# Kernel optimization log

Measured on AMD Instinct MI355X. Metric: run time of the kernel, lower is better.

## Reference

```python
import jax, jax.numpy as jnp
import numpy as np

B, T, D = 2, 1024, 2048
N, K, H = 16, 4, 128          # num_heads, num_kv_heads, head_dim
TC = 1024                     # cached tokens
S = TC + T
MAX_WAVELENGTH = 10000.0
BIG_NEG = -2.3819763e38


def _apply_rope(x, positions):
    """RoPE: positions [B,L] applied to x [B,L,heads,H]."""
    half = x.shape[-1] // 2
    freq_exponents = (2.0 / x.shape[-1]) * jnp.arange(half, dtype=jnp.float32)
    timescale = MAX_WAVELENGTH ** freq_exponents                      # [H/2]
    radians = (positions.astype(jnp.float32)[..., None] / timescale)[..., None, :]  # [B,L,1,H/2]
    sin, cos = jnp.sin(radians), jnp.cos(radians)
    x1, x2 = jnp.split(x, 2, axis=-1)
    res = jnp.concatenate([x1 * cos - x2 * sin, x2 * cos + x1 * sin], axis=-1)
    return res.astype(x.dtype)


def setup_inputs() -> dict:
    key = jax.random.key(0)
    ks = jax.random.split(key, 8)
    x = jax.random.normal(ks[0], (B, T, D), dtype=jnp.float32)
    # new tokens sit right after the cache
    positions = jnp.broadcast_to(TC + jnp.arange(T, dtype=jnp.int32), (B, T))
    # causal mask over [cache + new]: query t may attend to keys s <= TC + t
    s_idx = jnp.arange(S)[None, :]
    t_idx = jnp.arange(T)[:, None]
    attn_mask = jnp.broadcast_to((s_idx <= TC + t_idx)[None, None, :, :], (B, 1, T, S))
    cache_k = jax.random.normal(ks[1], (B, TC, K, H), dtype=jnp.float32)
    cache_v = jax.random.normal(ks[2], (B, TC, K, H), dtype=jnp.float32)
    # lecun-normal-ish fan-in scaling (fan_in = D for projections, N*H for output)
    w_q = jax.random.normal(ks[3], (N, D, H), dtype=jnp.float32) * (D ** -0.5)
    w_kv = jax.random.normal(ks[4], (2, K, D, H), dtype=jnp.float32) * (D ** -0.5)
    w_out = jax.random.normal(ks[5], (N, H, D), dtype=jnp.float32) * ((N * H) ** -0.5)
    return {"x": x, "positions": positions, "attn_mask": attn_mask,
            "cache_k": cache_k, "cache_v": cache_v,
            "w_q": w_q, "w_kv": w_kv, "w_out": w_out}


def reference(x, positions, attn_mask, cache_k, cache_v, w_q, w_kv, w_out):
    dtype = x.dtype
    # projections (GQA path: num_kv_heads != num_heads)
    q = jnp.einsum('BTD,NDH->BTNH', x, w_q.astype(dtype))
    kv = jnp.einsum('BSD,CKDH->CBSKH', x, w_kv.astype(dtype))
    k_new, v_new = kv[0], kv[1]
    # inline RoPE + query scaling
    q = _apply_rope(q, positions) * (H ** -0.5)
    k_new = _apply_rope(k_new, positions)
    # KV-cache concat
    k = jnp.concatenate([cache_k, k_new], axis=1)   # [B,S,K,H]
    v = jnp.concatenate([cache_v, v_new], axis=1)
    # group heads: B T (K G) H -> B T K G H
    G = N // K
    qg = q.reshape(q.shape[0], q.shape[1], K, G, H)
    logits = jnp.einsum('BTKGH,BSKH->BKGTS', qg, k,
                        preferred_element_type=jnp.float32)
    masked = jnp.where(attn_mask[:, :, None, :, :], logits, BIG_NEG)
    probs = jax.nn.softmax(masked, axis=-1).astype(dtype)
    enc = jnp.einsum('BKGTS,BSKH->BTKGH', probs, v)
    enc = enc.reshape(enc.shape[0], enc.shape[1], N, H)  # B T (K G) H
    out = jnp.einsum('BTNH,NHD->BTD', enc, w_out.astype(dtype))
    return out, k, v
```

## Files before the change

### kernel.cpp

```cpp
#include <hip/hip_runtime.h>

#define B_  2
#define T_  1024
#define D_  2048
#define NH  16
#define KH  4
#define HD  128
#define TC_ 1024
#define S_  2048

typedef __bf16 bf16x4v __attribute__((ext_vector_type(4)));
typedef __bf16 bf16x8v __attribute__((ext_vector_type(8)));
typedef float  f32x4v  __attribute__((ext_vector_type(4)));

__device__ __forceinline__ void async_copy16(void* lds, const void* g) {
    __builtin_amdgcn_global_load_lds(
        (__attribute__((address_space(1))) void*)g,
        (__attribute__((address_space(3))) void*)lds, 16, 0, 0);
}

__global__ void cvt_x(const float* __restrict__ x, __bf16* __restrict__ xb) {
    int i = (blockIdx.x * 256 + threadIdx.x) * 4;
    float4 v = *(const float4*)(x + i);
    bf16x4v o; o[0]=(__bf16)v.x; o[1]=(__bf16)v.y; o[2]=(__bf16)v.z; o[3]=(__bf16)v.w;
    *(bf16x4v*)(xb + i) = o;
}

__global__ void tp_w(const float* __restrict__ in, __bf16* __restrict__ out) {
    __shared__ float tile[32][33];
    int h0 = blockIdx.x * 32;
    int d0 = blockIdx.y * 32;
    const float* ip = in + (size_t)blockIdx.z * (D_ * HD);
    __bf16* op = out + (size_t)blockIdx.z * (D_ * HD);
    int tx = threadIdx.x, ty = threadIdx.y;
    for (int i = 0; i < 32; i += 8)
        tile[ty + i][tx] = ip[(size_t)(d0 + ty + i) * HD + h0 + tx];
    __syncthreads();
    for (int i = 0; i < 32; i += 8)
        op[(size_t)(h0 + ty + i) * D_ + d0 + tx] = (__bf16)tile[tx][ty + i];
}

__global__ void tp_wout(const float* __restrict__ in, __bf16* __restrict__ out) {
    __shared__ float tile[32][33];
    int d0 = blockIdx.x * 32;
    int h0 = blockIdx.y * 32;
    int n  = blockIdx.z;
    const float* ip = in + (size_t)n * (HD * D_);
    int tx = threadIdx.x, ty = threadIdx.y;
    for (int i = 0; i < 32; i += 8)
        tile[ty + i][tx] = ip[(size_t)(h0 + ty + i) * D_ + d0 + tx];
    __syncthreads();
    for (int i = 0; i < 32; i += 8)
        out[(size_t)(d0 + ty + i) * (NH * HD) + n * HD + h0 + tx] = (__bf16)tile[tx][ty + i];
}

__global__ void tp_v(const float* __restrict__ vout, __bf16* __restrict__ vtb) {
    __shared__ float tile[32][33];
    int z = blockIdx.z; int b = z / KH, kh = z % KH;
    int h0 = blockIdx.x * 32;
    int s0 = blockIdx.y * 32;
    const float* ip = vout + ((size_t)b * S_ * KH + kh) * HD;
    int tx = threadIdx.x, ty = threadIdx.y;
    for (int i = 0; i < 32; i += 8)
        tile[ty + i][tx] = ip[(size_t)(s0 + ty + i) * (KH * HD) + h0 + tx];
    __syncthreads();
    __bf16* op = vtb + ((size_t)b * KH + kh) * (size_t)HD * S_;
    for (int i = 0; i < 32; i += 8)
        op[(size_t)(h0 + ty + i) * S_ + s0 + tx] = (__bf16)tile[tx][ty + i];
}

__global__ void copy_cache(const float4* __restrict__ ck, const float4* __restrict__ cv,
                           float* __restrict__ kout, float* __restrict__ vout,
                           __bf16* __restrict__ kb) {
    int i = blockIdx.x * 256 + threadIdx.x;
    int b = i >> 17;
    int r = i & 131071;
    float4 kv = ck[i];
    ((float4*)(kout + (size_t)b * S_ * KH * HD))[r] = kv;
    ((float4*)(vout + (size_t)b * S_ * KH * HD))[r] = cv[i];
    int h4 = r & 31;
    int kh = (r >> 5) & 3;
    int s  = r >> 7;
    bf16x4v o; o[0]=(__bf16)kv.x; o[1]=(__bf16)kv.y; o[2]=(__bf16)kv.z; o[3]=(__bf16)kv.w;
    *(bf16x4v*)(kb + (((size_t)(b * KH + kh) * S_ + s) * HD) + h4 * 4) = o;
}

__global__ __launch_bounds__(256, 2)
void gemm_qkv(const __bf16* __restrict__ A, const __bf16* __restrict__ BT,
              const int* __restrict__ pos, __bf16* __restrict__ qws,
              float* __restrict__ kout, float* __restrict__ vout,
              __bf16* __restrict__ kb) {
    __shared__ __bf16 As[128 * 64];
    __shared__ __bf16 Bs[128 * 64];
    const int m0 = blockIdx.x * 128, n0 = blockIdx.y * 128;
    const int tid = threadIdx.x;
    const int wave = tid >> 6, lane = tid & 63;
    const int quad = lane >> 4, l16 = lane & 15;
    const int wm = (wave & 1) * 64;
    const int bn0 = (wave >> 1) * 32;
    const int lrow = lane >> 3;
    const int lsw  = (lane & 7) ^ (lrow & 7);

    f32x4v acc[4][4];
    for (int i = 0; i < 4; i++)
        for (int j = 0; j < 4; j++)
            acc[i][j] = (f32x4v){0.f, 0.f, 0.f, 0.f};

    const __bf16* Abase = A + (size_t)m0 * D_;
    const __bf16* Bbase = BT + (size_t)n0 * D_;

    for (int k0 = 0; k0 < D_; k0 += 64) {
        for (int j = 0; j < 4; j++) {
            int r = wave * 32 + j * 8;
            async_copy16(As + (size_t)r * 64,
                         Abase + (size_t)(r + lrow) * D_ + k0 + lsw * 8);
            async_copy16(Bs + (size_t)r * 64,
                         Bbase + (size_t)(r + lrow) * D_ + k0 + lsw * 8);
        }
        __syncthreads();
        for (int ks = 0; ks < 2; ks++) {
            const int ch = ((ks * 4 + quad) ^ (l16 & 7)) * 8;
            bf16x8v a[4], b[4];
            for (int i = 0; i < 4; i++)
                a[i] = *(const bf16x8v*)(As + (wm + i * 16 + l16) * 64 + ch);
            for (int j = 0; j < 4; j++) {
                int bn = bn0 + (j >> 1) * 16 + (j & 1) * 64;
                b[j] = *(const bf16x8v*)(Bs + (bn + l16) * 64 + ch);
            }
            for (int i = 0; i < 4; i++)
                for (int j = 0; j < 4; j++)
                    acc[i][j] = __builtin_amdgcn_mfma_f32_16x16x32_bf16(a[i], b[j], acc[i][j], 0, 0, 0);
        }
        __syncthreads();
    }

    const float RFREQ = 9.210340371976184f / 64.0f;
    const float qscale = 0.08838834764831845f;
    const int head = blockIdx.y;

    if (head < NH) {
        for (int i = 0; i < 4; i++)
            for (int r = 0; r < 4; r++) {
                int row = m0 + wm + i * 16 + quad * 4 + r;
                float p = (float)pos[row];
                size_t qo = ((size_t)row * NH + head) * HD;
                for (int jp = 0; jp < 2; jp++) {
                    int hh = bn0 + jp * 16 + l16;
                    float ang = p * __expf(-(float)hh * RFREQ);
                    float sn, cs; __sincosf(ang, &sn, &cs);
                    float x1 = acc[i][jp * 2][r], x2 = acc[i][jp * 2 + 1][r];
                    qws[qo + hh]      = (__bf16)((x1 * cs - x2 * sn) * qscale);
                    qws[qo + hh + 64] = (__bf16)((x2 * cs + x1 * sn) * qscale);
                }
            }
    } else if (head < NH + KH) {
        int kh = head - NH;
        for (int i = 0; i < 4; i++)
            for (int r = 0; r < 4; r++) {
                int row = m0 + wm + i * 16 + quad * 4 + r;
                int b = row >> 10, t = row & 1023;
                float p = (float)pos[row];
                size_t ko  = ((size_t)(b * S_ + TC_ + t) * KH + kh) * HD;
                size_t kbo = ((size_t)(b * KH + kh) * S_ + TC_ + t) * HD;
                for (int jp = 0; jp < 2; jp++) {
                    int hh = bn0 + jp * 16 + l16;
                    float ang = p * __expf(-(float)hh * RFREQ);
                    float sn, cs; __sincosf(ang, &sn, &cs);
                    float x1 = acc[i][jp * 2][r], x2 = acc[i][jp * 2 + 1][r];
                    float k1 = x1 * cs - x2 * sn, k2 = x2 * cs + x1 * sn;
                    kout[ko + hh]      = k1;
                    kout[ko + hh + 64] = k2;
                    kb[kbo + hh]      = (__bf16)k1;
                    kb[kbo + hh + 64] = (__bf16)k2;
                }
            }
    } else {
        int kh = head - NH - KH;
        for (int i = 0; i < 4; i++)
            for (int r = 0; r < 4; r++) {
                int row = m0 + wm + i * 16 + quad * 4 + r;
                int b = row >> 10, t = row & 1023;
                size_t vo = ((size_t)(b * S_ + TC_ + t) * KH + kh) * HD;
                for (int j = 0; j < 4; j++) {
                    int h = bn0 + (j >> 1) * 16 + (j & 1) * 64 + l16;
                    vout[vo + h] = acc[i][j][r];
                }
            }
    }
}

__global__ __launch_bounds__(256, 2)
void gemm_bt(const __bf16* __restrict__ A, const __bf16* __restrict__ BT,
             float* __restrict__ C0, float* __restrict__ C1, int ldc, int kchunk) {
    __shared__ __bf16 As[128 * 64];
    __shared__ __bf16 Bs[128 * 64];
    const int m0 = blockIdx.x * 128, n0 = blockIdx.y * 128;
    const int kbeg = blockIdx.z * kchunk;
    float* C = blockIdx.z ? C1 : C0;
    const int tid = threadIdx.x;
    const int wave = tid >> 6, lane = tid & 63;
    const int quad = lane >> 4, l16 = lane & 15;
    const int wm = (wave & 1) * 64, wn = (wave >> 1) * 64;
    const int lrow = lane >> 3;
    const int lsw  = (lane & 7) ^ (lrow & 7);

    f32x4v acc[4][4];
    for (int i = 0; i < 4; i++)
        for (int j = 0; j < 4; j++)
            acc[i][j] = (f32x4v){0.f, 0.f, 0.f, 0.f};

    const __bf16* Abase = A + (size_t)m0 * D_;
    const __bf16* Bbase = BT + (size_t)n0 * D_;

    for (int k0 = kbeg; k0 < kbeg + kchunk; k0 += 64) {
        for (int j = 0; j < 4; j++) {
            int r = wave * 32 + j * 8;
            async_copy16(As + (size_t)r * 64,
                         Abase + (size_t)(r + lrow) * D_ + k0 + lsw * 8);
            async_copy16(Bs + (size_t)r * 64,
                         Bbase + (size_t)(r + lrow) * D_ + k0 + lsw * 8);
        }
        __syncthreads();
        for (int ks = 0; ks < 2; ks++) {
            const int ch = ((ks * 4 + quad) ^ (l16 & 7)) * 8;
            bf16x8v a[4], b[4];
            for (int i = 0; i < 4; i++)
                a[i] = *(const bf16x8v*)(As + (wm + i * 16 + l16) * 64 + ch);
            for (int j = 0; j < 4; j++)
                b[j] = *(const bf16x8v*)(Bs + (wn + j * 16 + l16) * 64 + ch);
            for (int i = 0; i < 4; i++)
                for (int j = 0; j < 4; j++)
                    acc[i][j] = __builtin_amdgcn_mfma_f32_16x16x32_bf16(a[i], b[j], acc[i][j], 0, 0, 0);
        }
        __syncthreads();
    }
    for (int i = 0; i < 4; i++)
        for (int j = 0; j < 4; j++)
            for (int r = 0; r < 4; r++) {
                int row = m0 + wm + i * 16 + quad * 4 + r;
                int col = n0 + wn + j * 16 + l16;
                C[(size_t)row * ldc + col] = acc[i][j][r];
            }
}

__global__ void add2(float* __restrict__ out, const float* __restrict__ p1) {
    int i = blockIdx.x * 256 + threadIdx.x;
    f32x4v a = *(const f32x4v*)(out + (size_t)i * 4);
    f32x4v b = *(const f32x4v*)(p1 + (size_t)i * 4);
    a[0]+=b[0]; a[1]+=b[1]; a[2]+=b[2]; a[3]+=b[3];
    *(f32x4v*)(out + (size_t)i * 4) = a;
}

__global__ __launch_bounds__(512, 1)
void attn(const __bf16* __restrict__ qws, const __bf16* __restrict__ kb,
          const __bf16* __restrict__ vtb, __bf16* __restrict__ enc) {
    __shared__ __bf16 Qs[128 * 128];
    __shared__ __bf16 Ks[128 * 128];
    __shared__ __bf16 Vs[128 * 128];
    __shared__ __bf16 Ps[128 * 128];

    const int t0 = blockIdx.x * 128;
    const int n  = blockIdx.y;
    const int b  = blockIdx.z;
    const int kh = n / (NH / KH);
    const int tid = threadIdx.x, wave = tid >> 6, lane = tid & 63;
    const int quad = lane >> 4, l16 = lane & 15;
    const int wm = wave * 16;
    const int arow = lane >> 4;
    const int acol = lane & 15;

    {
        const __bf16* qtile = qws + ((size_t)(b * T_ + t0) * NH + n) * HD;
        for (int jj = 0; jj < 4; jj++) {
            int r0 = wm + jj * 4;
            int row = r0 + arow;
            async_copy16(Qs + (size_t)r0 * 128,
                         qtile + (size_t)row * (NH * HD) + ((acol ^ (row & 15)) * 8));
        }
    }

    float m_run[4], l_run[4];
    f32x4v o_acc[8];
    for (int r = 0; r < 4; r++) { m_run[r] = -INFINITY; l_run[r] = 0.f; }
    for (int j = 0; j < 8; j++) o_acc[j] = (f32x4v){0.f, 0.f, 0.f, 0.f};

    const int nS = (TC_ + t0 + 128) >> 7;
    const __bf16* kbase = kb  + ((size_t)(b * KH + kh)) * S_ * HD;
    const __bf16* vbase = vtb + ((size_t)(b * KH + kh)) * (size_t)HD * S_;

    for (int st = 0; st < nS; st++) {
        const int s0 = st * 128;
        {
            const __bf16* ktile = kbase + (size_t)s0 * HD;
            for (int jj = 0; jj < 4; jj++) {
                int r0 = wm + jj * 4;
                int row = r0 + arow;
                async_copy16(Ks + (size_t)r0 * 128,
                             ktile + (size_t)row * HD + ((acol ^ (row & 15)) * 8));
            }
        }
        {
            const __bf16* vtile = vbase + s0;
            for (int jj = 0; jj < 4; jj++) {
                int r0 = wm + jj * 4;
                int row = r0 + arow;
                async_copy16(Vs + (size_t)r0 * 128,
                             vtile + (size_t)row * S_ + ((acol ^ (row & 15)) * 8));
            }
        }
        __syncthreads();

        f32x4v sc[8];
        for (int j = 0; j < 8; j++) sc[j] = (f32x4v){0.f, 0.f, 0.f, 0.f};
        for (int ks = 0; ks < 4; ks++) {
            int ch = (ks * 4 + quad) ^ l16;
            bf16x8v a = *(const bf16x8v*)(Qs + (wm + l16) * 128 + ch * 8);
            bf16x8v bb[8];
            for (int j = 0; j < 8; j++)
                bb[j] = *(const bf16x8v*)(Ks + (j * 16 + l16) * 128 + ch * 8);
            for (int j = 0; j < 8; j++)
                sc[j] = __builtin_amdgcn_mfma_f32_16x16x32_bf16(a, bb[j], sc[j], 0, 0, 0);
        }

        if (st == nS - 1) {
            for (int j = 0; j < 8; j++)
                for (int r = 0; r < 4; r++) {
                    int row = wm + quad * 4 + r;
                    int col = j * 16 + l16;
                    if (col > row) sc[j][r] = -3.0e38f;
                }
        }

        for (int r = 0; r < 4; r++) {
            float mx = sc[0][r];
            for (int j = 1; j < 8; j++) mx = fmaxf(mx, sc[j][r]);
            for (int off = 8; off >= 1; off >>= 1) mx = fmaxf(mx, __shfl_xor(mx, off, 64));
            mx = fmaxf(mx, m_run[r]);
            float alpha = __expf(m_run[r] - mx);
            m_run[r] = mx;
            float s = 0.f;
            for (int j = 0; j < 8; j++) {
                float pv = __expf(sc[j][r] - mx);
                sc[j][r] = pv;
                s += pv;
            }
            for (int off = 8; off >= 1; off >>= 1) s += __shfl_xor(s, off, 64);
            l_run[r] = l_run[r] * alpha + s;
            for (int j = 0; j < 8; j++) o_acc[j][r] *= alpha;
        }

        for (int j = 0; j < 8; j++)
            for (int r = 0; r < 4; r++) {
                int row = wm + quad * 4 + r;
                int c = (j * 2 + (l16 >> 3)) ^ (row & 15);
                Ps[row * 128 + c * 8 + (l16 & 7)] = (__bf16)sc[j][r];
            }
        __syncthreads();

        for (int ks = 0; ks < 4; ks++) {
            int ch = (ks * 4 + quad) ^ l16;
            bf16x8v a = *(const bf16x8v*)(Ps + (wm + l16) * 128 + ch * 8);
            bf16x8v bb[8];
            for (int j = 0; j < 8; j++)
                bb[j] = *(const bf16x8v*)(Vs + (j * 16 + l16) * 128 + ch * 8);
            for (int j = 0; j < 8; j++)
                o_acc[j] = __builtin_amdgcn_mfma_f32_16x16x32_bf16(a, bb[j], o_acc[j], 0, 0, 0);
        }
        __syncthreads();
    }

    for (int r = 0; r < 4; r++) {
        float inv = 1.0f / l_run[r];
        int row = wm + quad * 4 + r;
        for (int j = 0; j < 8; j++) {
            int col = j * 16 + l16;
            enc[((size_t)(b * T_ + t0 + row) * NH + n) * HD + col] =
                (__bf16)(o_acc[j][r] * inv);
        }
    }
}

extern "C" void kernel_launch(void* const* d_in, const int* in_sizes, int n_in,
                              void* d_out, int out_size, void* d_ws, size_t ws_size,
                              hipStream_t stream) {
    const float* x       = (const float*)d_in[0];
    const int*   pos     = (const int*)d_in[1];
    const float* cache_k = (const float*)d_in[3];
    const float* cache_v = (const float*)d_in[4];
    const float* w_q     = (const float*)d_in[5];
    const float* w_kv    = (const float*)d_in[6];
    const float* w_out   = (const float*)d_in[7];

    float* out  = (float*)d_out;
    float* kout = out  + (size_t)B_ * T_ * D_;
    float* vout = kout + (size_t)B_ * S_ * KH * HD;

    char* ws = (char*)d_ws;
    __bf16* xb   = (__bf16*)ws;  ws += (size_t)B_ * T_ * D_ * 2;
    __bf16* wt   = (__bf16*)ws;  ws += (size_t)3072 * D_ * 2;
    __bf16* wot  = (__bf16*)ws;  ws += (size_t)D_ * NH * HD * 2;
    float*  op1  = (float*)ws;   ws += (size_t)B_ * T_ * D_ * 4;
    __bf16* qws  = (__bf16*)ws;  ws += (size_t)B_ * T_ * NH * HD * 2;
    __bf16* kbuf = (__bf16*)ws;  ws += (size_t)B_ * S_ * KH * HD * 2;
    __bf16* vtb  = (__bf16*)ws;  ws += (size_t)B_ * S_ * KH * HD * 2;
    __bf16* enc  = (__bf16*)ws;

    cvt_x<<<4096, 256, 0, stream>>>(x, xb);
    tp_w<<<dim3(4, 64, 16), dim3(32, 8), 0, stream>>>(w_q, wt);
    tp_w<<<dim3(4, 64, 8),  dim3(32, 8), 0, stream>>>(w_kv, wt + (size_t)16 * HD * D_);
    tp_wout<<<dim3(64, 4, 16), dim3(32, 8), 0, stream>>>(w_out, wot);
    copy_cache<<<1024, 256, 0, stream>>>((const float4*)cache_k, (const float4*)cache_v, kout, vout, kbuf);
    gemm_qkv<<<dim3(16, 24), 256, 0, stream>>>(xb, wt, pos, qws, kout, vout, kbuf);
    tp_v<<<dim3(4, 64, 8), dim3(32, 8), 0, stream>>>(vout, vtb);
    attn<<<dim3(8, 16, 2), 512, 0, stream>>>(qws, kbuf, vtb, enc);
    gemm_bt<<<dim3(16, 16, 2), 256, 0, stream>>>(enc, wot, out, op1, 2048, 1024);
    add2<<<4096, 256, 0, stream>>>(out, op1);
}
```

Measured before the change: 274.4 us.

## Merge prep kernels, drop split-K output GEMM, add lazy softmax rescaling

```diff
diff --git a/kernel.cpp b/kernel.cpp
--- a/kernel.cpp
+++ b/kernel.cpp
@@ -19,39 +19,63 @@
         (__attribute__((address_space(3))) void*)lds, 16, 0, 0);
 }
 
-__global__ void cvt_x(const float* __restrict__ x, __bf16* __restrict__ xb) {
-    int i = (blockIdx.x * 256 + threadIdx.x) * 4;
-    float4 v = *(const float4*)(x + i);
-    bf16x4v o; o[0]=(__bf16)v.x; o[1]=(__bf16)v.y; o[2]=(__bf16)v.z; o[3]=(__bf16)v.w;
-    *(bf16x4v*)(xb + i) = o;
-}
-
-__global__ void tp_w(const float* __restrict__ in, __bf16* __restrict__ out) {
+__global__ void prep(const float* __restrict__ x, __bf16* __restrict__ xb,
+                     const float4* __restrict__ ck, const float4* __restrict__ cv,
+                     float* __restrict__ kout, float* __restrict__ vout,
+                     __bf16* __restrict__ kb) {
+    int bid = blockIdx.x;
+    if (bid < 4096) {
+        int i = (bid * 256 + threadIdx.x) * 4;
+        float4 v = *(const float4*)(x + i);
+        bf16x4v o; o[0]=(__bf16)v.x; o[1]=(__bf16)v.y; o[2]=(__bf16)v.z; o[3]=(__bf16)v.w;
+        *(bf16x4v*)(xb + i) = o;
+    } else {
+        int i = (bid - 4096) * 256 + threadIdx.x;
+        int b = i >> 17;
+        int r = i & 131071;
+        float4 kv = ck[i];
+        ((float4*)(kout + (size_t)b * S_ * KH * HD))[r] = kv;
+        ((float4*)(vout + (size_t)b * S_ * KH * HD))[r] = cv[i];
+        int h4 = r & 31;
+        int kh = (r >> 5) & 3;
+        int s  = r >> 7;
+        bf16x4v o; o[0]=(__bf16)kv.x; o[1]=(__bf16)kv.y; o[2]=(__bf16)kv.z; o[3]=(__bf16)kv.w;
+        *(bf16x4v*)(kb + (((size_t)(b * KH + kh) * S_ + s) * HD) + h4 * 4) = o;
+    }
+}
+
+__global__ void tp_all(const float* __restrict__ wq, const float* __restrict__ wkv,
+                       const float* __restrict__ wo, __bf16* __restrict__ wt,
+                       __bf16* __restrict__ wot) {
     __shared__ float tile[32][33];
-    int h0 = blockIdx.x * 32;
-    int d0 = blockIdx.y * 32;
-    const float* ip = in + (size_t)blockIdx.z * (D_ * HD);
-    __bf16* op = out + (size_t)blockIdx.z * (D_ * HD);
+    int bid = blockIdx.x;
     int tx = threadIdx.x, ty = threadIdx.y;
-    for (int i = 0; i < 32; i += 8)
-        tile[ty + i][tx] = ip[(size_t)(d0 + ty + i) * HD + h0 + tx];
-    __syncthreads();
-    for (int i = 0; i < 32; i += 8)
-        op[(size_t)(h0 + ty + i) * D_ + d0 + tx] = (__bf16)tile[tx][ty + i];
-}
-
-__global__ void tp_wout(const float* __restrict__ in, __bf16* __restrict__ out) {
-    __shared__ float tile[32][33];
-    int d0 = blockIdx.x * 32;
-    int h0 = blockIdx.y * 32;
-    int n  = blockIdx.z;
-    const float* ip = in + (size_t)n * (HD * D_);
-    int tx = threadIdx.x, ty = threadIdx.y;
-    for (int i = 0; i < 32; i += 8)
-        tile[ty + i][tx] = ip[(size_t)(h0 + ty + i) * D_ + d0 + tx];
-    __syncthreads();
-    for (int i = 0; i < 32; i += 8)
-        out[(size_t)(d0 + ty + i) * (NH * HD) + n * HD + h0 + tx] = (__bf16)tile[tx][ty + i];
+    if (bid < 6144) {
+        int zz  = bid >> 8;
+        int rem = bid & 255;
+        int h0 = (rem & 3) * 32;
+        int d0 = (rem >> 2) * 32;
+        const float* ip = (zz < 16) ? (wq + (size_t)zz * D_ * HD)
+                                    : (wkv + (size_t)(zz - 16) * D_ * HD);
+        __bf16* op = wt + (size_t)zz * D_ * HD;
+        for (int i = 0; i < 32; i += 8)
+            tile[ty + i][tx] = ip[(size_t)(d0 + ty + i) * HD + h0 + tx];
+        __syncthreads();
+        for (int i = 0; i < 32; i += 8)
+            op[(size_t)(h0 + ty + i) * D_ + d0 + tx] = (__bf16)tile[tx][ty + i];
+    } else {
+        int r2  = bid - 6144;
+        int n   = r2 >> 8;
+        int rem = r2 & 255;
+        int d0 = (rem & 63) * 32;
+        int h0 = (rem >> 6) * 32;
+        const float* ip = wo + (size_t)n * (HD * D_);
+        for (int i = 0; i < 32; i += 8)
+            tile[ty + i][tx] = ip[(size_t)(h0 + ty + i) * D_ + d0 + tx];
+        __syncthreads();
+        for (int i = 0; i < 32; i += 8)
+            wot[(size_t)(d0 + ty + i) * (NH * HD) + n * HD + h0 + tx] = (__bf16)tile[tx][ty + i];
+    }
 }
 
 __global__ void tp_v(const float* __restrict__ vout, __bf16* __restrict__ vtb) {
@@ -67,22 +91,6 @@
     __bf16* op = vtb + ((size_t)b * KH + kh) * (size_t)HD * S_;
     for (int i = 0; i < 32; i += 8)
         op[(size_t)(h0 + ty + i) * S_ + s0 + tx] = (__bf16)tile[tx][ty + i];
-}
-
-__global__ void copy_cache(const float4* __restrict__ ck, const float4* __restrict__ cv,
-                           float* __restrict__ kout, float* __restrict__ vout,
-                           __bf16* __restrict__ kb) {
-    int i = blockIdx.x * 256 + threadIdx.x;
-    int b = i >> 17;
-    int r = i & 131071;
-    float4 kv = ck[i];
-    ((float4*)(kout + (size_t)b * S_ * KH * HD))[r] = kv;
-    ((float4*)(vout + (size_t)b * S_ * KH * HD))[r] = cv[i];
-    int h4 = r & 31;
-    int kh = (r >> 5) & 3;
-    int s  = r >> 7;
-    bf16x4v o; o[0]=(__bf16)kv.x; o[1]=(__bf16)kv.y; o[2]=(__bf16)kv.z; o[3]=(__bf16)kv.w;
-    *(bf16x4v*)(kb + (((size_t)(b * KH + kh) * S_ + s) * HD) + h4 * 4) = o;
 }
 
 __global__ __launch_bounds__(256, 2)
@@ -191,12 +199,10 @@
 
 __global__ __launch_bounds__(256, 2)
 void gemm_bt(const __bf16* __restrict__ A, const __bf16* __restrict__ BT,
-             float* __restrict__ C0, float* __restrict__ C1, int ldc, int kchunk) {
+             float* __restrict__ C, int ldc) {
     __shared__ __bf16 As[128 * 64];
     __shared__ __bf16 Bs[128 * 64];
     const int m0 = blockIdx.x * 128, n0 = blockIdx.y * 128;
-    const int kbeg = blockIdx.z * kchunk;
-    float* C = blockIdx.z ? C1 : C0;
     const int tid = threadIdx.x;
     const int wave = tid >> 6, lane = tid & 63;
     const int quad = lane >> 4, l16 = lane & 15;
@@ -212,7 +218,7 @@
     const __bf16* Abase = A + (size_t)m0 * D_;
     const __bf16* Bbase = BT + (size_t)n0 * D_;
 
-    for (int k0 = kbeg; k0 < kbeg + kchunk; k0 += 64) {
+    for (int k0 = 0; k0 < D_; k0 += 64) {
         for (int j = 0; j < 4; j++) {
             int r = wave * 32 + j * 8;
             async_copy16(As + (size_t)r * 64,
@@ -243,14 +249,6 @@
             }
 }
 
-__global__ void add2(float* __restrict__ out, const float* __restrict__ p1) {
-    int i = blockIdx.x * 256 + threadIdx.x;
-    f32x4v a = *(const f32x4v*)(out + (size_t)i * 4);
-    f32x4v b = *(const f32x4v*)(p1 + (size_t)i * 4);
-    a[0]+=b[0]; a[1]+=b[1]; a[2]+=b[2]; a[3]+=b[3];
-    *(f32x4v*)(out + (size_t)i * 4) = a;
-}
-
 __global__ __launch_bounds__(512, 1)
 void attn(const __bf16* __restrict__ qws, const __bf16* __restrict__ kb,
           const __bf16* __restrict__ vtb, __bf16* __restrict__ enc) {
@@ -335,18 +333,24 @@
             float mx = sc[0][r];
             for (int j = 1; j < 8; j++) mx = fmaxf(mx, sc[j][r]);
             for (int off = 8; off >= 1; off >>= 1) mx = fmaxf(mx, __shfl_xor(mx, off, 64));
-            mx = fmaxf(mx, m_run[r]);
-            float alpha = __expf(m_run[r] - mx);
-            m_run[r] = mx;
+            float m;
+            if (mx > m_run[r] + 8.f) {
+                m = mx;
+                float alpha = __expf(m_run[r] - mx);
+                for (int j = 0; j < 8; j++) o_acc[j][r] *= alpha;
+                l_run[r] *= alpha;
+                m_run[r] = m;
+            } else {
+                m = m_run[r];
+            }
             float s = 0.f;
             for (int j = 0; j < 8; j++) {
-                float pv = __expf(sc[j][r] - mx);
+                float pv = __expf(sc[j][r] - m);
                 sc[j][r] = pv;
                 s += pv;
             }
             for (int off = 8; off >= 1; off >>= 1) s += __shfl_xor(s, off, 64);
-            l_run[r] = l_run[r] * alpha + s;
-            for (int j = 0; j < 8; j++) o_acc[j][r] *= alpha;
+            l_run[r] += s;
         }
 
         for (int j = 0; j < 8; j++)
@@ -399,20 +403,16 @@
     __bf16* xb   = (__bf16*)ws;  ws += (size_t)B_ * T_ * D_ * 2;
     __bf16* wt   = (__bf16*)ws;  ws += (size_t)3072 * D_ * 2;
     __bf16* wot  = (__bf16*)ws;  ws += (size_t)D_ * NH * HD * 2;
-    float*  op1  = (float*)ws;   ws += (size_t)B_ * T_ * D_ * 4;
     __bf16* qws  = (__bf16*)ws;  ws += (size_t)B_ * T_ * NH * HD * 2;
     __bf16* kbuf = (__bf16*)ws;  ws += (size_t)B_ * S_ * KH * HD * 2;
     __bf16* vtb  = (__bf16*)ws;  ws += (size_t)B_ * S_ * KH * HD * 2;
     __bf16* enc  = (__bf16*)ws;
 
-    cvt_x<<<4096, 256, 0, stream>>>(x, xb);
-    tp_w<<<dim3(4, 64, 16), dim3(32, 8), 0, stream>>>(w_q, wt);
-    tp_w<<<dim3(4, 64, 8),  dim3(32, 8), 0, stream>>>(w_kv, wt + (size_t)16 * HD * D_);
-    tp_wout<<<dim3(64, 4, 16), dim3(32, 8), 0, stream>>>(w_out, wot);
-    copy_cache<<<1024, 256, 0, stream>>>((const float4*)cache_k, (const float4*)cache_v, kout, vout, kbuf);
+    prep<<<5120, 256, 0, stream>>>(x, xb, (const float4*)cache_k, (const float4*)cache_v,
+                                   kout, vout, kbuf);
+    tp_all<<<10240, dim3(32, 8), 0, stream>>>(w_q, w_kv, w_out, wt, wot);
     gemm_qkv<<<dim3(16, 24), 256, 0, stream>>>(xb, wt, pos, qws, kout, vout, kbuf);
     tp_v<<<dim3(4, 64, 8), dim3(32, 8), 0, stream>>>(vout, vtb);
     attn<<<dim3(8, 16, 2), 512, 0, stream>>>(qws, kbuf, vtb, enc);
-    gemm_bt<<<dim3(16, 16, 2), 256, 0, stream>>>(enc, wot, out, op1, 2048, 1024);
-    add2<<<4096, 256, 0, stream>>>(out, op1);
-}
+    gemm_bt<<<dim3(16, 16), 256, 0, stream>>>(enc, wot, out, 2048);
+}
```

After: 275.5 us. Within noise of the previous version (+0.4%).
